# Optimization experiments

Measured on AMD Instinct MI355X. Metric: run time of the kernel, lower is better.

The kernel has to match this reference:

```python
import jax, jax.numpy as jnp
import numpy as np

B, T, DIM = 2, 2048, 1024
H, HD = 16, 64          # num_heads, head_dim (DIM = H*HD)
SCALE = 0.12            # fixed attn_scale in the module
ROPE_BASE = 1024.0
EPS = 1e-6


def _rope_tables(seq_len, head_dim):
    half = head_dim // 2
    keep = head_dim // 4
    active = (1.0 / ROPE_BASE) ** jnp.linspace(0.0, 1.0, keep, dtype=jnp.float32)
    inv_freq = jnp.concatenate([active, jnp.zeros(half - keep, dtype=jnp.float32)])
    theta = jnp.arange(seq_len, dtype=jnp.float32)[:, None] * inv_freq[None, :]  # [T, half]
    return jnp.cos(theta), jnp.sin(theta)


def _rms_norm(x):
    # F.rms_norm without learned scale
    return x * jax.lax.rsqrt(jnp.mean(x * x, axis=-1, keepdims=True) + EPS)


def _apply_rope(x_bthd, cos, sin):
    # x_bthd: [B,T,H,HD]; cos/sin: [T, HD/2]
    xf = x_bthd.astype(jnp.float32)
    x1, x2 = jnp.split(xf, 2, axis=-1)
    c = cos[None, :, None, :]
    s = sin[None, :, None, :]
    y = jnp.concatenate([x1 * c + x2 * s, -x1 * s + x2 * c], axis=-1)
    return y.astype(x_bthd.dtype)


def setup_inputs() -> dict:
    key = jax.random.key(0)
    k1, k2, k3, k4 = jax.random.split(key, 4)
    x = jax.random.normal(k1, (B, T, DIM), dtype=jnp.float32)
    ve = jax.random.normal(k2, (B, T, DIM), dtype=jnp.float32)
    sa_lambdas = jax.random.uniform(k3, (2,), dtype=jnp.float32)
    # additive causal mask, as SDPA receives a float mask cast to q dtype
    causal = jnp.tril(jnp.ones((T, T), dtype=bool))
    attn_mask = jnp.where(causal, 0.0, -1e9).astype(jnp.float32)[None, None]
    # qkvo weights; scaled like a typical linear init (original zero-inits W_o,
    # here kept random so the output is non-trivial for kernel testing)
    qkvo_w = jax.random.normal(k4, (4, DIM, DIM), dtype=jnp.float32) * (DIM ** -0.5)
    return {"x": x, "ve": ve, "sa_lambdas": sa_lambdas, "attn_mask": attn_mask, "qkvo_w": qkvo_w}


def reference(x, ve, sa_lambdas, attn_mask, qkvo_w):
    b, t, _ = x.shape
    # fused QKV projection: qkvo_w[:3] is [3, DIM, DIM], F.linear -> x @ W.T
    qkv = jnp.einsum('btd,ked->btke', x, qkvo_w[:3])          # [B,T,3,DIM]
    q = _rms_norm(qkv[:, :, 0].reshape(b, t, H, HD))
    k = _rms_norm(qkv[:, :, 1].reshape(b, t, H, HD))
    v = _rms_norm(qkv[:, :, 2].reshape(b, t, H, HD))
    cos, sin = _rope_tables(t, HD)
    q = _apply_rope(q, cos, sin)
    k = _apply_rope(k, cos, sin)
    # value-embedding blend
    v = sa_lambdas[0] * v + sa_lambdas[1] * ve.reshape(b, t, H, HD)
    # attention with fixed scale and additive mask
    scores = jnp.einsum('bthd,bshd->bhts', q, k) * SCALE + attn_mask
    att = jax.nn.softmax(scores, axis=-1)
    y = jnp.einsum('bhts,bshd->bthd', att, v).reshape(b, t, DIM)
    return y @ qkvo_w[3].T
```

## Files before the change

### kernel.cpp

```cpp
#include <hip/hip_runtime.h>
#include <hip/hip_bf16.h>
#include <stdint.h>

#define T_SEQ 2048
#define DIMSZ 1024
#define NH    16
#define HDIM  64
#define NBATCH 2
#define KVB   64
#define ATT_SCALE 0.12f
#define QSCALE (0.12f * 1.4426950408889634f)

typedef __attribute__((ext_vector_type(8))) __bf16 bf16x8;
typedef __attribute__((ext_vector_type(8))) ushort u16x8;
typedef __attribute__((ext_vector_type(4))) float f32x4;

#define GLOAD_LDS16(gp, lp)                                                            \
  __builtin_amdgcn_global_load_lds((const __attribute__((address_space(1))) void*)(gp),\
                                   (__attribute__((address_space(3))) void*)(lp),      \
                                   16, 0, 0)

__device__ __forceinline__ ushort f2bf(float f) {
  union { float f; uint32_t u; } v; v.f = f;
  uint32_t u = v.u;
  uint32_t r = (u + 0x7FFFu + ((u >> 16) & 1u)) >> 16;
  return (ushort)r;
}

__device__ __forceinline__ float bf2f(ushort h) {
  union { float f; uint32_t u; } v;
  v.u = ((uint32_t)h) << 16;
  return v.f;
}

__device__ __forceinline__ uint32_t pk2(float a, float b) {
  union { __hip_bfloat162 h; uint32_t u; } cv;
  cv.h = __hip_bfloat162(__float2bfloat16(a), __float2bfloat16(b));
  return cv.u;
}

__global__ __launch_bounds__(256) void conv_bf16_k(const float* __restrict__ in,
                                                   ushort* __restrict__ out, int n) {
  int i = (blockIdx.x * 256 + threadIdx.x) * 4;
  if (i >= n) return;
  float4 v = *(const float4*)(in + i);
  ushort4 o;
  o.x = f2bf(v.x); o.y = f2bf(v.y); o.z = f2bf(v.z); o.w = f2bf(v.w);
  *(ushort4*)(out + i) = o;
}

__global__ __launch_bounds__(256) void rope_tab_k(float* __restrict__ ctab,
                                                  float* __restrict__ stab) {
  int idx = blockIdx.x * 256 + threadIdx.x;
  if (idx >= T_SEQ * 32) return;
  int j = idx & 31, t = idx >> 5;
  float c = 1.f, s = 0.f;
  if (j < 16) {
    float inv = powf(1024.0f, -(float)j / 15.0f);
    float th = (float)t * inv;
    c = cosf(th);
    s = sinf(th);
  }
  ctab[idx] = c;
  stab[idx] = s;
}

#define BM 128
#define BN 128
#define BKS 64

template <typename OT>
__global__ __launch_bounds__(256) void gemm_bt_k(const ushort* __restrict__ A,
                                                 const ushort* __restrict__ Bt,
                                                 OT* __restrict__ C,
                                                 int M, int N, int K) {
  __shared__ __align__(16) ushort As[BM * BKS];
  __shared__ __align__(16) ushort Bs[BN * BKS];
  int tid = threadIdx.x;
  int wave = tid >> 6, lane = tid & 63;
  int lr = lane & 15, lg = lane >> 4;
  int m0 = blockIdx.x * BM, n0 = blockIdx.y * BN;
  int wm = (wave >> 1) * 64, wn = (wave & 1) * 64;

  f32x4 acc[4][4];
  for (int m = 0; m < 4; ++m)
    for (int n = 0; n < 4; ++n)
      acc[m][n] = (f32x4){0.f, 0.f, 0.f, 0.f};

  for (int k0 = 0; k0 < K; k0 += BKS) {
#pragma unroll
    for (int it = 0; it < 4; ++it) {
      int idx = it * 256 + tid;
      int row = idx >> 3;
      int col = (idx & 7) * 8;
      GLOAD_LDS16(A + (size_t)(m0 + row) * K + k0 + col, &As[idx * 8]);
      GLOAD_LDS16(Bt + (size_t)(n0 + row) * K + k0 + col, &Bs[idx * 8]);
    }
    __syncthreads();
#pragma unroll
    for (int kk = 0; kk < 2; ++kk) {
      bf16x8 af[4], bf[4];
#pragma unroll
      for (int m = 0; m < 4; ++m)
        af[m] = *(const bf16x8*)&As[(wm + m * 16 + lr) * BKS + kk * 32 + lg * 8];
#pragma unroll
      for (int n = 0; n < 4; ++n)
        bf[n] = *(const bf16x8*)&Bs[(wn + n * 16 + lr) * BKS + kk * 32 + lg * 8];
#pragma unroll
      for (int m = 0; m < 4; ++m)
#pragma unroll
        for (int n = 0; n < 4; ++n)
          acc[m][n] = __builtin_amdgcn_mfma_f32_16x16x32_bf16(af[m], bf[n], acc[m][n], 0, 0, 0);
    }
    __syncthreads();
  }
#pragma unroll
  for (int m = 0; m < 4; ++m)
#pragma unroll
    for (int n = 0; n < 4; ++n)
#pragma unroll
      for (int r = 0; r < 4; ++r) {
        int row = m0 + wm + m * 16 + lg * 4 + r;
        int col = n0 + wn + n * 16 + lr;
        if constexpr (sizeof(OT) == 2)
          C[(size_t)row * N + col] = (OT)f2bf(acc[m][n][r]);
        else
          C[(size_t)row * N + col] = (OT)acc[m][n][r];
      }
}

#define BM2 256
#define BN2 256

__global__ __launch_bounds__(512, 2) void gemm_qkv_k(const ushort* __restrict__ A,
                                                     const ushort* __restrict__ Bt,
                                                     const float* __restrict__ ve,
                                                     const float* __restrict__ lam,
                                                     const float* __restrict__ ctab,
                                                     const float* __restrict__ stab,
                                                     ushort* __restrict__ Qb,
                                                     ushort* __restrict__ Kb,
                                                     ushort* __restrict__ Vt) {
  const int K = DIMSZ;
  __shared__ __align__(16) ushort As[2][BM2 * BKS];
  __shared__ __align__(16) ushort Bs[2][BN2 * BKS];
  int tid = threadIdx.x;
  int wid = tid >> 6, lane = tid & 63;
  int lr = lane & 15, lg = lane >> 4;
  int m0 = blockIdx.x * BM2, n0 = blockIdx.y * BN2;
  int wm = (wid >> 2) * 128, wn = (wid & 3) * 64;

  int srow = tid >> 3;
  int sel = (((tid & 7) ^ (srow & 7)) << 3);
  const ushort* aSrc = A + (size_t)(m0 + srow) * K + sel;
  const ushort* bSrc = Bt + (size_t)(n0 + srow) * K + sel;
  int dstoff = tid * 8;

  f32x4 acc[8][4];
#pragma unroll
  for (int m = 0; m < 8; ++m)
#pragma unroll
    for (int n = 0; n < 4; ++n)
      acc[m][n] = (f32x4){0.f, 0.f, 0.f, 0.f};

#pragma unroll
  for (int it = 0; it < 4; ++it) {
    GLOAD_LDS16(aSrc + (size_t)it * 64 * K, &As[0][it * 4096 + dstoff]);
    GLOAD_LDS16(bSrc + (size_t)it * 64 * K, &Bs[0][it * 4096 + dstoff]);
  }

  int rs = lr & 7;
  for (int ks = 0; ks < 16; ++ks) {
    int cur = ks & 1;
    if (ks + 1 < 16) {
      int k0 = (ks + 1) * BKS;
#pragma unroll
      for (int it = 0; it < 4; ++it) {
        GLOAD_LDS16(aSrc + (size_t)it * 64 * K + k0, &As[cur ^ 1][it * 4096 + dstoff]);
        GLOAD_LDS16(bSrc + (size_t)it * 64 * K + k0, &Bs[cur ^ 1][it * 4096 + dstoff]);
      }
      asm volatile("s_waitcnt vmcnt(8)" ::: "memory");
    } else {
      asm volatile("s_waitcnt vmcnt(0)" ::: "memory");
    }
    __builtin_amdgcn_s_barrier();
    __builtin_amdgcn_sched_barrier(0);
    const ushort* Ac = &As[cur][0];
    const ushort* Bc = &Bs[cur][0];
#pragma unroll
    for (int kk = 0; kk < 2; ++kk) {
      int cA = (((kk * 4 + lg) ^ rs) << 3);
      bf16x8 af[8], bfr[4];
#pragma unroll
      for (int m = 0; m < 8; ++m)
        af[m] = *(const bf16x8*)&Ac[(wm + m * 16 + lr) * 64 + cA];
#pragma unroll
      for (int n = 0; n < 4; ++n)
        bfr[n] = *(const bf16x8*)&Bc[(wn + n * 16 + lr) * 64 + cA];
#pragma unroll
      for (int m = 0; m < 8; ++m)
#pragma unroll
        for (int n = 0; n < 4; ++n)
          acc[m][n] = __builtin_amdgcn_mfma_f32_16x16x32_bf16(af[m], bfr[n], acc[m][n], 0, 0, 0);
    }
    __builtin_amdgcn_sched_barrier(0);
    __builtin_amdgcn_s_barrier();
  }
  __syncthreads();

  int sec = n0 >> 10;
  int h = ((n0 & 1023) + wn) >> 6;
  ushort* Tl = &As[0][0] + wid * 4096;
  float l0 = lam[0], l1 = lam[1];

#pragma unroll
  for (int hf = 0; hf < 2; ++hf) {
#pragma unroll
    for (int mi = 0; mi < 4; ++mi)
#pragma unroll
      for (int n = 0; n < 4; ++n)
#pragma unroll
        for (int r = 0; r < 4; ++r) {
          int tl = mi * 16 + lg * 4 + r;
          int d = n * 16 + lr;
          Tl[tl * 64 + ((((d >> 3) ^ (tl & 7)) << 3) | (d & 7))] = f2bf(acc[hf * 4 + mi][n][r]);
        }
    int tl = lane;
    float xv[64];
#pragma unroll
    for (int j = 0; j < 8; ++j) {
      u16x8 rw = *(const u16x8*)&Tl[tl * 64 + ((j ^ (tl & 7)) << 3)];
#pragma unroll
      for (int e = 0; e < 8; ++e) xv[j * 8 + e] = bf2f((ushort)rw[e]);
    }
    float ss = 0.f;
#pragma unroll
    for (int i = 0; i < 64; ++i) ss += xv[i] * xv[i];
    float rinv = rsqrtf(ss * (1.0f / 64.0f) + 1e-6f);
#pragma unroll
    for (int i = 0; i < 64; ++i) xv[i] *= rinv;

    int row = m0 + wm + hf * 64 + tl;
    int t = row & (T_SEQ - 1);
    int bb = row >> 11;
    int bh = bb * NH + h;

    if (sec < 2) {
      float cs[16], sn[16];
      const float4* cp = (const float4*)(ctab + t * 32);
      const float4* sp = (const float4*)(stab + t * 32);
#pragma unroll
      for (int j = 0; j < 4; ++j) {
        float4 c4 = cp[j], s4 = sp[j];
        cs[j * 4 + 0] = c4.x; cs[j * 4 + 1] = c4.y; cs[j * 4 + 2] = c4.z; cs[j * 4 + 3] = c4.w;
        sn[j * 4 + 0] = s4.x; sn[j * 4 + 1] = s4.y; sn[j * 4 + 2] = s4.z; sn[j * 4 + 3] = s4.w;
      }
#pragma unroll
      for (int j = 0; j < 16; ++j) {
        float a = xv[j], bv = xv[j + 32];
        xv[j] = a * cs[j] + bv * sn[j];
        xv[j + 32] = bv * cs[j] - a * sn[j];
      }
      float sc = (sec == 0) ? QSCALE : 1.0f;
      ushort* dst = (sec == 0 ? Qb : Kb) + ((size_t)bh * T_SEQ + t) * HDIM;
#pragma unroll
      for (int p = 0; p < 8; ++p) {
        uint4 wq = make_uint4(pk2(xv[8 * p] * sc, xv[8 * p + 1] * sc),
                              pk2(xv[8 * p + 2] * sc, xv[8 * p + 3] * sc),
                              pk2(xv[8 * p + 4] * sc, xv[8 * p + 5] * sc),
                              pk2(xv[8 * p + 6] * sc, xv[8 * p + 7] * sc));
        *((uint4*)dst + p) = wq;
      }
    } else {
      const float4* vp = (const float4*)(ve + ((size_t)(bb * T_SEQ + t)) * DIMSZ + h * HDIM);
#pragma unroll
      for (int j = 0; j < 16; ++j) {
        float4 vv4 = vp[j];
        xv[j * 4 + 0] = l0 * xv[j * 4 + 0] + l1 * vv4.x;
        xv[j * 4 + 1] = l0 * xv[j * 4 + 1] + l1 * vv4.y;
        xv[j * 4 + 2] = l0 * xv[j * 4 + 2] + l1 * vv4.z;
        xv[j * 4 + 3] = l0 * xv[j * 4 + 3] + l1 * vv4.w;
      }
      ushort* dst = Vt + (size_t)bh * HDIM * T_SEQ + t;
#pragma unroll
      for (int i = 0; i < 64; ++i)
        dst[(size_t)i * T_SEQ] = f2bf(xv[i]);
    }
  }
}

__global__ __launch_bounds__(512, 4) void attn_k(const ushort* __restrict__ Q,
                                                 const ushort* __restrict__ K,
                                                 const ushort* __restrict__ Vt,
                                                 ushort* __restrict__ Y) {
  int bh = blockIdx.x;
  int pair = blockIdx.y;
  int tid = threadIdx.x;
  int wid = tid >> 6, lane = tid & 63;
  int lr = lane & 15, lg = lane >> 4;
  int b = bh >> 4, h = bh & 15;

  int NT = 32 - pair;
  int grp = wid >> 2;
  int myqb = grp ? (31 - pair) : pair;
  int mylast = grp ? (NT - 1) : pair;
  int strip = wid & 3;
  int r0 = myqb * 64 + strip * 16;

  __shared__ __align__(16) ushort Kl[2][KVB * HDIM];
  __shared__ __align__(16) ushort Vl[2][KVB * HDIM];
  __shared__ __align__(16) ushort Plds[8][16][72];

  const ushort* Kbh = K + (size_t)bh * T_SEQ * HDIM;
  const ushort* Vbh = Vt + (size_t)bh * HDIM * T_SEQ;

  int srow = tid >> 3, schunk = tid & 7;
  int sel = ((schunk ^ (srow & 7)) << 3);
  const ushort* ksrc = Kbh + (size_t)srow * HDIM + sel;
  const ushort* vsrc = Vbh + (size_t)srow * T_SEQ + sel;
  int ldst = wid << 9;

  const ushort* Qbase = Q + ((size_t)bh * T_SEQ + r0) * HDIM;
  bf16x8 aq[2];
#pragma unroll
  for (int kk = 0; kk < 2; ++kk)
    aq[kk] = *(const bf16x8*)(Qbase + (size_t)lr * HDIM + kk * 32 + lg * 8);

  int fcol[2];
  fcol[0] = ((0 + lg) ^ (lr & 7)) << 3;
  fcol[1] = ((4 + lg) ^ (lr & 7)) << 3;

  f32x4 o[4];
#pragma unroll
  for (int n = 0; n < 4; ++n) o[n] = (f32x4){0.f, 0.f, 0.f, 0.f};
  float lrow = 0.f;

  GLOAD_LDS16(ksrc, &Kl[0][ldst]);
  GLOAD_LDS16(vsrc, &Vl[0][ldst]);
  __syncthreads();

  int cur = 0;
  for (int kb = 0; kb < NT; ++kb) {
    if (kb + 1 < NT) {
      GLOAD_LDS16(ksrc + (size_t)(kb + 1) * KVB * HDIM, &Kl[cur ^ 1][ldst]);
      GLOAD_LDS16(vsrc + (kb + 1) * KVB, &Vl[cur ^ 1][ldst]);
    }
    if (kb <= mylast) {
      const ushort* Kc = &Kl[cur][0];
      const ushort* Vc = &Vl[cur][0];
      f32x4 s[4];
#pragma unroll
      for (int n = 0; n < 4; ++n) {
        f32x4 a = (f32x4){0.f, 0.f, 0.f, 0.f};
        bf16x8 kf0 = *(const bf16x8*)&Kc[(n * 16 + lr) * HDIM + fcol[0]];
        a = __builtin_amdgcn_mfma_f32_16x16x32_bf16(kf0, aq[0], a, 0, 0, 0);
        bf16x8 kf1 = *(const bf16x8*)&Kc[(n * 16 + lr) * HDIM + fcol[1]];
        a = __builtin_amdgcn_mfma_f32_16x16x32_bf16(kf1, aq[1], a, 0, 0, 0);
        s[n] = a;
      }
      if (kb == mylast) {
        int qrow = r0 + lr;
        int kb0 = kb * KVB + lg * 4;
#pragma unroll
        for (int n = 0; n < 4; ++n)
#pragma unroll
          for (int r = 0; r < 4; ++r)
            if (kb0 + n * 16 + r > qrow) s[n][r] = -1e30f;
      }
      float psum = 0.f;
#pragma unroll
      for (int n = 0; n < 4; ++n) {
        float p0 = exp2f(s[n][0]), p1 = exp2f(s[n][1]);
        float p2 = exp2f(s[n][2]), p3 = exp2f(s[n][3]);
        psum += (p0 + p1) + (p2 + p3);
        uint2 w;
        w.x = pk2(p0, p1);
        w.y = pk2(p2, p3);
        *(uint2*)&Plds[wid][lr][n * 16 + lg * 4] = w;
      }
      lrow += psum;
#pragma unroll
      for (int kk = 0; kk < 2; ++kk) {
        bf16x8 ap = *(const bf16x8*)&Plds[wid][lr][kk * 32 + lg * 8];
#pragma unroll
        for (int n = 0; n < 4; ++n) {
          bf16x8 vf = *(const bf16x8*)&Vc[(n * 16 + lr) * HDIM + fcol[kk]];
          o[n] = __builtin_amdgcn_mfma_f32_16x16x32_bf16(vf, ap, o[n], 0, 0, 0);
        }
      }
    }
    __syncthreads();
    cur ^= 1;
  }
  lrow += __shfl_xor(lrow, 16);
  lrow += __shfl_xor(lrow, 32);
  float inv = 1.0f / lrow;
  int row = r0 + lr;
#pragma unroll
  for (int n = 0; n < 4; ++n) {
    uint2 w;
    w.x = pk2(o[n][0] * inv, o[n][1] * inv);
    w.y = pk2(o[n][2] * inv, o[n][3] * inv);
    *(uint2*)&Y[((size_t)b * T_SEQ + row) * DIMSZ + h * HDIM + n * 16 + lg * 4] = w;
  }
}

extern "C" void kernel_launch(void* const* d_in, const int* in_sizes, int n_in,
                              void* d_out, int out_size, void* d_ws, size_t ws_size,
                              hipStream_t stream) {
  const float* x   = (const float*)d_in[0];
  const float* ve  = (const float*)d_in[1];
  const float* lam = (const float*)d_in[2];
  const float* w   = (const float*)d_in[4];
  float* out = (float*)d_out;

  char* ws = (char*)d_ws;
  const size_t NTOK = (size_t)NBATCH * T_SEQ;
  const size_t nX = NTOK * DIMSZ;
  const size_t nW = 4ull * DIMSZ * DIMSZ;

  ushort* Xb   = (ushort*)(ws);
  ushort* Wb   = (ushort*)(ws + 8388608);
  ushort* Qb   = (ushort*)(ws + 16777216);
  ushort* Kb   = (ushort*)(ws + 25165824);
  ushort* Vt   = (ushort*)(ws + 33554432);
  ushort* Yb   = (ushort*)(ws + 41943040);
  float*  ctab = (float*)(ws + 50331648);
  float*  stab = (float*)(ws + 50593792);

  conv_bf16_k<<<(int)(nX / 4 / 256), 256, 0, stream>>>(x, Xb, (int)nX);
  conv_bf16_k<<<(int)(nW / 4 / 256), 256, 0, stream>>>(w, Wb, (int)nW);
  rope_tab_k<<<(T_SEQ * 32) / 256, 256, 0, stream>>>(ctab, stab);

  gemm_qkv_k<<<dim3(4096 / BM2, 3072 / BN2), 512, 0, stream>>>(Xb, Wb, ve, lam, ctab, stab,
                                                               Qb, Kb, Vt);

  attn_k<<<dim3(NBATCH * NH, 16), 512, 0, stream>>>(Qb, Kb, Vt, Yb);

  gemm_bt_k<float><<<dim3(4096 / BM, 1024 / BN), 256, 0, stream>>>(Yb, Wb + 3ull * DIMSZ * DIMSZ, out, 4096, 1024, 1024);
}
```

Before: 134.8 us.

## Interleave QKV GEMM prefetch chunks with MFMA quads and raise priority

Restructures the QKV GEMM main loop so each k-step is split into four MFMA quads, with the next tile's global-to-LDS loads issued in pieces between quads instead of all at the top. Wait counts and barriers are rearranged so B and A halves are prefetched at staggered points, and s_setprio wraps MFMA bursts to favor compute. B fragments are loaded once per step for both k sub-steps. The aim is better overlap of memory traffic with MFMA and fewer exposed stalls, at the cost of more barriers per iteration and fragile hand-tuned vmcnt accounting.

```diff
diff --git a/kernel.cpp b/kernel.cpp
--- a/kernel.cpp
+++ b/kernel.cpp
@@ -132,6 +132,22 @@
 #define BM2 256
 #define BN2 256
 
+#define QUAD(p)                                                                        \
+  {                                                                                    \
+    bf16x8 af[2][2];                                                                   \
+    _Pragma("unroll") for (int i = 0; i < 2; ++i)                                      \
+      _Pragma("unroll") for (int kk = 0; kk < 2; ++kk)                                 \
+        af[i][kk] = *(const bf16x8*)&Ac[(wm + (2 * (p) + i) * 16 + lr) * 64 +          \
+                                        (((kk * 4 + lg) ^ rs) << 3)];                  \
+    __builtin_amdgcn_s_setprio(1);                                                     \
+    _Pragma("unroll") for (int i = 0; i < 2; ++i)                                      \
+      _Pragma("unroll") for (int kk = 0; kk < 2; ++kk)                                 \
+        _Pragma("unroll") for (int n = 0; n < 4; ++n)                                  \
+          acc[2 * (p) + i][n] = __builtin_amdgcn_mfma_f32_16x16x32_bf16(               \
+              af[i][kk], bfr[n][kk], acc[2 * (p) + i][n], 0, 0, 0);                    \
+    __builtin_amdgcn_s_setprio(0);                                                     \
+  }
+
 __global__ __launch_bounds__(512, 2) void gemm_qkv_k(const ushort* __restrict__ A,
                                                      const ushort* __restrict__ Bt,
                                                      const float* __restrict__ ve,
@@ -142,13 +158,14 @@
                                                      ushort* __restrict__ Kb,
                                                      ushort* __restrict__ Vt) {
   const int K = DIMSZ;
-  __shared__ __align__(16) ushort As[2][BM2 * BKS];
-  __shared__ __align__(16) ushort Bs[2][BN2 * BKS];
+  __shared__ __align__(16) ushort Ab[2][BM2 * BKS];
+  __shared__ __align__(16) ushort Bb[2][BN2 * BKS];
   int tid = threadIdx.x;
   int wid = tid >> 6, lane = tid & 63;
   int lr = lane & 15, lg = lane >> 4;
   int m0 = blockIdx.x * BM2, n0 = blockIdx.y * BN2;
   int wm = (wid >> 2) * 128, wn = (wid & 3) * 64;
+  int rs = lr & 7;
 
   int srow = tid >> 3;
   int sel = (((tid & 7) ^ (srow & 7)) << 3);
@@ -163,54 +180,71 @@
     for (int n = 0; n < 4; ++n)
       acc[m][n] = (f32x4){0.f, 0.f, 0.f, 0.f};
 
-#pragma unroll
-  for (int it = 0; it < 4; ++it) {
-    GLOAD_LDS16(aSrc + (size_t)it * 64 * K, &As[0][it * 4096 + dstoff]);
-    GLOAD_LDS16(bSrc + (size_t)it * 64 * K, &Bs[0][it * 4096 + dstoff]);
-  }
-
-  int rs = lr & 7;
-  for (int ks = 0; ks < 16; ++ks) {
-    int cur = ks & 1;
-    if (ks + 1 < 16) {
-      int k0 = (ks + 1) * BKS;
-#pragma unroll
-      for (int it = 0; it < 4; ++it) {
-        GLOAD_LDS16(aSrc + (size_t)it * 64 * K + k0, &As[cur ^ 1][it * 4096 + dstoff]);
-        GLOAD_LDS16(bSrc + (size_t)it * 64 * K + k0, &Bs[cur ^ 1][it * 4096 + dstoff]);
-      }
-      asm volatile("s_waitcnt vmcnt(8)" ::: "memory");
+  GLOAD_LDS16(bSrc + 0 * 64 * K, &Bb[0][0 * 4096 + dstoff]);
+  GLOAD_LDS16(bSrc + 1 * 64 * K, &Bb[0][1 * 4096 + dstoff]);
+  GLOAD_LDS16(bSrc + 2 * 64 * K, &Bb[0][2 * 4096 + dstoff]);
+  GLOAD_LDS16(bSrc + 3 * 64 * K, &Bb[0][3 * 4096 + dstoff]);
+  GLOAD_LDS16(aSrc + 0 * 64 * K, &Ab[0][0 * 4096 + dstoff]);
+  GLOAD_LDS16(aSrc + 2 * 64 * K, &Ab[0][2 * 4096 + dstoff]);
+  GLOAD_LDS16(aSrc + 1 * 64 * K, &Ab[0][1 * 4096 + dstoff]);
+  GLOAD_LDS16(aSrc + 3 * 64 * K, &Ab[0][3 * 4096 + dstoff]);
+
+  bf16x8 bfr[4][2];
+
+  for (int T = 0; T < 16; ++T) {
+    const int cur = T & 1;
+    const ushort* Ac = &Ab[cur][0];
+    const ushort* Bc = &Bb[cur][0];
+    ushort* An = &Ab[cur ^ 1][0];
+    ushort* Bn = &Bb[cur ^ 1][0];
+    const bool pre = (T + 1 < 16);
+    const int k1 = (T + 1) * BKS;
+
+    asm volatile("s_waitcnt vmcnt(2)" ::: "memory");
+    __builtin_amdgcn_s_barrier();
+    asm volatile("" ::: "memory");
+    if (pre) {
+      GLOAD_LDS16(bSrc + (size_t)0 * 64 * K + k1, &Bn[0 * 4096 + dstoff]);
+      GLOAD_LDS16(bSrc + (size_t)1 * 64 * K + k1, &Bn[1 * 4096 + dstoff]);
+    }
+#pragma unroll
+    for (int n = 0; n < 4; ++n)
+#pragma unroll
+      for (int kk = 0; kk < 2; ++kk)
+        bfr[n][kk] = *(const bf16x8*)&Bc[(wn + n * 16 + lr) * 64 + (((kk * 4 + lg) ^ rs) << 3)];
+    QUAD(0);
+    __builtin_amdgcn_s_barrier();
+    asm volatile("" ::: "memory");
+    if (pre) {
+      GLOAD_LDS16(bSrc + (size_t)2 * 64 * K + k1, &Bn[2 * 4096 + dstoff]);
+      GLOAD_LDS16(bSrc + (size_t)3 * 64 * K + k1, &Bn[3 * 4096 + dstoff]);
+    }
+    QUAD(1);
+    if (pre) {
+      asm volatile("s_waitcnt vmcnt(4)" ::: "memory");
     } else {
       asm volatile("s_waitcnt vmcnt(0)" ::: "memory");
     }
     __builtin_amdgcn_s_barrier();
-    __builtin_amdgcn_sched_barrier(0);
-    const ushort* Ac = &As[cur][0];
-    const ushort* Bc = &Bs[cur][0];
-#pragma unroll
-    for (int kk = 0; kk < 2; ++kk) {
-      int cA = (((kk * 4 + lg) ^ rs) << 3);
-      bf16x8 af[8], bfr[4];
-#pragma unroll
-      for (int m = 0; m < 8; ++m)
-        af[m] = *(const bf16x8*)&Ac[(wm + m * 16 + lr) * 64 + cA];
-#pragma unroll
-      for (int n = 0; n < 4; ++n)
-        bfr[n] = *(const bf16x8*)&Bc[(wn + n * 16 + lr) * 64 + cA];
-#pragma unroll
-      for (int m = 0; m < 8; ++m)
-#pragma unroll
-        for (int n = 0; n < 4; ++n)
-          acc[m][n] = __builtin_amdgcn_mfma_f32_16x16x32_bf16(af[m], bfr[n], acc[m][n], 0, 0, 0);
-    }
-    __builtin_amdgcn_sched_barrier(0);
+    asm volatile("" ::: "memory");
+    if (pre) {
+      GLOAD_LDS16(aSrc + (size_t)0 * 64 * K + k1, &An[0 * 4096 + dstoff]);
+      GLOAD_LDS16(aSrc + (size_t)2 * 64 * K + k1, &An[2 * 4096 + dstoff]);
+    }
+    QUAD(2);
     __builtin_amdgcn_s_barrier();
+    asm volatile("" ::: "memory");
+    if (pre) {
+      GLOAD_LDS16(aSrc + (size_t)1 * 64 * K + k1, &An[1 * 4096 + dstoff]);
+      GLOAD_LDS16(aSrc + (size_t)3 * 64 * K + k1, &An[3 * 4096 + dstoff]);
+    }
+    QUAD(3);
   }
   __syncthreads();
 
   int sec = n0 >> 10;
   int h = ((n0 & 1023) + wn) >> 6;
-  ushort* Tl = &As[0][0] + wid * 4096;
+  ushort* Tl = &Ab[0][0] + wid * 4096;
   float l0 = lam[0], l1 = lam[1];
 
 #pragma unroll
```

Result: slower. 146.5 us (+8.7%).
